# Kernel tuning notes

Hardware: AMD Instinct MI355X
Metric: run time of the kernel (lower is better)

The kernel has to match this reference:

```python
import jax, jax.numpy as jnp
import numpy as np

SEQ_LEN = 252
FEAT = 21
HID = 128


def setup_inputs() -> dict:
    key = jax.random.key(0)
    ks = jax.random.split(key, 20)
    B = 4096
    values = jax.random.normal(ks[0], (B, SEQ_LEN, FEAT), jnp.float32)
    masks = (jax.random.uniform(ks[1], (B, SEQ_LEN, FEAT)) < 0.8).astype(jnp.float32)
    deltas = jax.random.uniform(ks[2], (B, SEQ_LEN, FEAT), jnp.float32)
    evals = jax.random.normal(ks[3], (B, SEQ_LEN, FEAT), jnp.float32)
    eval_masks = (jax.random.uniform(ks[4], (B, SEQ_LEN, FEAT)) < 0.2).astype(jnp.float32)
    labels = jax.random.normal(ks[5], (B, 1), jnp.float32)
    is_train = (jax.random.uniform(ks[6], (B, 1)) < 0.8).astype(jnp.float32)
    sd = 1.0 / np.sqrt(HID)
    u = lambda k, sh, s: jax.random.uniform(k, sh, jnp.float32, -s, s)
    W_decay = u(ks[7], (HID, FEAT), sd)
    b_decay = u(ks[8], (HID,), sd)
    W_reg = u(ks[9], (FEAT, HID), sd)
    b_reg = u(ks[10], (FEAT,), sd)
    W_ih = u(ks[11], (4 * HID, 2 * FEAT), sd)
    W_hh = u(ks[12], (4 * HID, HID), sd)
    b_ih = u(ks[13], (4 * HID,), sd)
    b_hh = u(ks[14], (4 * HID,), sd)
    W_out = u(ks[15], (1, HID), sd)
    b_out = u(ks[16], (1,), sd)
    return dict(values=values, masks=masks, deltas=deltas, evals=evals,
                eval_masks=eval_masks, labels=labels, is_train=is_train,
                W_decay=W_decay, b_decay=b_decay, W_reg=W_reg, b_reg=b_reg,
                W_ih=W_ih, W_hh=W_hh, b_ih=b_ih, b_hh=b_hh,
                W_out=W_out, b_out=b_out)


def reference(values, masks, deltas, evals, eval_masks, labels, is_train,
              W_decay, b_decay, W_reg, b_reg, W_ih, W_hh, b_ih, b_hh,
              W_out, b_out):
    B = values.shape[0]
    impute_weight, label_weight = 1.0, 1.0
    # time-major [T,B,F] for scan
    xs = (jnp.swapaxes(values, 0, 1), jnp.swapaxes(masks, 0, 1),
          jnp.swapaxes(deltas, 0, 1))
    h0 = jnp.zeros((B, HID), values.dtype)
    c0 = jnp.zeros((B, HID), values.dtype)

    def step(carry, xt):
        h, c, x_loss = carry
        x, m, d = xt
        gamma = jnp.exp(-jax.nn.relu(d @ W_decay.T + b_decay))  # [B,HID]
        h = h * gamma
        x_h = h @ W_reg.T + b_reg                                # [B,FEAT]
        x_c = m * x + (1.0 - m) * x_h
        x_loss = x_loss + jnp.sum(jnp.abs(x - x_h) * m) / (jnp.sum(m) + 1e-5)
        inp = jnp.concatenate([x_c, m], axis=1)                  # [B,2*FEAT]
        gates = inp @ W_ih.T + b_ih + h @ W_hh.T + b_hh          # [B,4*HID]
        i, f, g, o = jnp.split(gates, 4, axis=1)
        c = jax.nn.sigmoid(f) * c + jax.nn.sigmoid(i) * jnp.tanh(g)
        h = jax.nn.sigmoid(o) * jnp.tanh(c)
        return (h, c, x_loss), x_c

    (h, c, x_loss), imp = jax.lax.scan(step, (h0, c0, jnp.float32(0.0)), xs)
    imputations = jnp.swapaxes(imp, 0, 1)                        # [B,T,FEAT]
    y_h = h @ W_out.T + b_out                                    # [B,1]
    y_loss = jnp.sum((y_h - labels) ** 2 * is_train) / (jnp.sum(is_train) + 1e-5)
    loss = x_loss * impute_weight + y_loss * label_weight
    return loss, y_h, imputations
```

## Files before the change

### kernel.cpp

```cpp
#include <hip/hip_runtime.h>
#include <math.h>


#define T_LEN 252
#define FEAT  21
#define HID   128
#define BTOT  4096
#define BT    16
#define NB    (BTOT / BT)
#define NTHR  512
#define LOG2E 1.44269504088896f

#define WS_WHH2   0
#define WS_RDEN   65536
#define WS_XL     65792
#define WS_YNUM   66048
#define WS_YDEN   66304

typedef __attribute__((ext_vector_type(8))) short s16x8;
typedef __attribute__((ext_vector_type(4))) float f32x4;

#define MFMA16(A, B, C) __builtin_amdgcn_mfma_f32_16x16x32_bf16((A), (B), (C), 0, 0, 0)

__device__ __forceinline__ float exp2_f(float x) { return __builtin_amdgcn_exp2f(x); }
__device__ __forceinline__ float rcp_f(float x)  { return __builtin_amdgcn_rcpf(x); }
__device__ __forceinline__ unsigned short to_bf16(float x) {
    unsigned int u = __float_as_uint(x);
    return (unsigned short)((u + 0x7FFFu + ((u >> 16) & 1u)) >> 16);
}
__device__ __forceinline__ unsigned short to_bf16f(float x) {
    return (unsigned short)((__float_as_uint(x) + 0x8000u) >> 16);
}

__global__ __launch_bounds__(1024) void rits_den(
    const float* __restrict__ masks, float* __restrict__ rden)
{
    const int t = blockIdx.x;
    const int tid = threadIdx.x;
    __shared__ float red[1024];
    float acc = 0.0f;
    if (tid < 48 * FEAT) {
        int r0 = tid / FEAT, f = tid - r0 * FEAT;
        for (int r = r0; r < BTOT; r += 48)
            acc += masks[r * (T_LEN * FEAT) + t * FEAT + f];
    }
    red[tid] = acc;
    __syncthreads();
    #pragma unroll
    for (int s = 512; s > 0; s >>= 1) {
        if (tid < s) red[tid] += red[tid + s];
        __syncthreads();
    }
    if (tid == 0) rden[t] = 1.0f / (red[0] + 1e-5f);
}

__global__ __launch_bounds__(256) void rits_fold(
    const float* __restrict__ W_ih, const float* __restrict__ W_hh,
    const float* __restrict__ W_reg, float* __restrict__ whh2)
{
    int idx = blockIdx.x * 256 + threadIdx.x;
    int j4 = idx >> 7, k = idx & (HID - 1);
    float acc = W_hh[j4 * HID + k];
    #pragma unroll
    for (int f = 0; f < FEAT; ++f)
        acc += W_ih[j4 * (2 * FEAT) + f] * W_reg[f * HID + k];
    whh2[idx] = acc;
}

__global__ __launch_bounds__(NTHR, 2) void rits_main(
    const float* __restrict__ values, const float* __restrict__ masks,
    const float* __restrict__ deltas,
    const float* __restrict__ labels, const float* __restrict__ is_train,
    const float* __restrict__ W_decay, const float* __restrict__ b_decay,
    const float* __restrict__ W_reg, const float* __restrict__ b_reg,
    const float* __restrict__ W_ih, const float* __restrict__ W_hh,
    const float* __restrict__ b_ih, const float* __restrict__ b_hh,
    const float* __restrict__ W_out, const float* __restrict__ b_out,
    const float* __restrict__ whh2, const float* __restrict__ rden,
    float* __restrict__ out_yh,
    float* __restrict__ out_imp,
    float* __restrict__ xlpart, float* __restrict__ wsynum, float* __restrict__ wsyden)
{
    const int tid  = threadIdx.x;
    const int blk  = blockIdx.x;
    const int bbase = blk * BT;
    const int l    = tid & 63;
    const int wv   = tid >> 6;
    const int cidx = l & 15;
    const int gidx = l >> 4;
    const int jh   = 16 * wv + cidx;

    __shared__ unsigned short ak_s[2][BT][200];
    __shared__ unsigned short d_s[2][BT][40];
    __shared__ float2 xm_s[2][BT][22];
    __shared__ float hfin_s[BT][HID + 4];
    __shared__ float rden_s[T_LEN];
    __shared__ float red_s[NTHR];

    for (int i = tid; i < 2 * BT * 200; i += NTHR) ((unsigned short*)ak_s)[i] = 0;
    for (int i = tid; i < 2 * BT * 40;  i += NTHR) ((unsigned short*)d_s)[i] = 0;
    if (tid < T_LEN) rden_s[tid] = rden[tid];

    s16x8 bfr_g[4][6];
    float bs_r[4];
    #pragma unroll
    for (int g = 0; g < 4; ++g) {
        const float sg = (g == 2) ? (2.0f * LOG2E) : LOG2E;
        const float* rh2 = whh2 + (g * HID + jh) * HID;
        const float* rih = W_ih + (g * HID + jh) * (2 * FEAT);
        #pragma unroll
        for (int s = 0; s < 6; ++s) {
            s16x8 fr;
            #pragma unroll
            for (int j = 0; j < 8; ++j) {
                int k = 32 * s + 8 * gidx + j;
                float w;
                if (k < HID)       w = rh2[k];
                else if (k < 160)  w = (k - 128 < FEAT) ? rih[k - 128] : 0.0f;
                else               w = (k - 160 < FEAT) ? rih[FEAT + (k - 160)] : 0.0f;
                fr[j] = (short)to_bf16(w * sg);
            }
            bfr_g[g][s] = fr;
        }
        float bb = b_ih[g * HID + jh] + b_hh[g * HID + jh];
        #pragma unroll
        for (int f = 0; f < FEAT; ++f) bb += rih[f] * b_reg[f];
        bs_r[g] = bb * sg;
    }
    s16x8 bfr_d;
    {
        const float* rw = W_decay + jh * FEAT;
        #pragma unroll
        for (int j = 0; j < 8; ++j) {
            int f = 8 * gidx + j;
            bfr_d[j] = (short)to_bf16(f < FEAT ? rw[f] * LOG2E : 0.0f);
        }
    }
    const float bd_r = b_decay[jh] * LOG2E;
    const int  fx  = 16 * wv + cidx;
    const bool fxv = (wv < 2) && (fx < FEAT);
    const int  fxc = fxv ? fx : 0;
    s16x8 bfr_r[4];
    #pragma unroll
    for (int s = 0; s < 4; ++s) {
        s16x8 fr;
        #pragma unroll
        for (int j = 0; j < 8; ++j) {
            int k = 32 * s + 8 * gidx + j;
            fr[j] = (short)to_bf16(fxv ? W_reg[fxc * HID + k] : 0.0f);
        }
        bfr_r[s] = fr;
    }
    const float br_r = fxv ? b_reg[fxc] : 0.0f;
    __syncthreads();

    const int st  = tid - 128;
    const bool stg = (st >= 0) && (st < BT * FEAT);
    const int rr = stg ? st / FEAT : 0;
    const int ff = stg ? (st - rr * FEAT) : 0;
    const int rowbase = (bbase + rr) * (T_LEN * FEAT) + ff;
    float nx = 0.f, nm = 0.f, nd = 0.f;
    if (stg) {
        float x0 = values[rowbase], m0 = masks[rowbase];
        xm_s[0][rr][ff] = make_float2(x0, m0);
        ak_s[0][rr][160 + ff] = to_bf16(m0);
        nx = values[rowbase + FEAT];
        nm = masks[rowbase + FEAT];
        nd = deltas[rowbase + FEAT];
    }
    const int ibase = (bbase + 4 * gidx) * (T_LEN * FEAT) + fxc;
    float c_r[4]   = {0.f, 0.f, 0.f, 0.f};
    float h_r[4]   = {0.f, 0.f, 0.f, 0.f};
    float gam_r[4] = {0.f, 0.f, 0.f, 0.f};
    float xl_acc = 0.0f;
    __syncthreads();

    for (int t = 0; t < T_LEN; ++t) {
        const int par = t & 1;

        float lx = 0.f, lm = 0.f, ld = 0.f;
        if (stg) {
            d_s[par ^ 1][rr][ff] = to_bf16f(nd);
            xm_s[par ^ 1][rr][ff] = make_float2(nx, nm);
            int idx = (t + 2 < T_LEN) ? (t + 2) : (T_LEN - 1);
            int o = rowbase + idx * FEAT;
            lx = values[o]; lm = masks[o]; ld = deltas[o];
        }
        #pragma unroll
        for (int v = 0; v < 4; ++v)
            ak_s[par][4 * gidx + v][jh] = to_bf16f(h_r[v] * gam_r[v]);
        __syncthreads();

        s16x8 aF0 = *(const s16x8*)&ak_s[par][cidx][      8 * gidx];
        s16x8 aF1 = *(const s16x8*)&ak_s[par][cidx][ 32 + 8 * gidx];
        s16x8 aF2 = *(const s16x8*)&ak_s[par][cidx][ 64 + 8 * gidx];
        s16x8 aF3 = *(const s16x8*)&ak_s[par][cidx][ 96 + 8 * gidx];
        s16x8 aM  = *(const s16x8*)&ak_s[par][cidx][160 + 8 * gidx];
        s16x8 ad  = *(const s16x8*)&d_s[par ^ 1][cidx][8 * gidx];
        if (stg) ak_s[par ^ 1][rr][160 + ff] = to_bf16f(nm);

        f32x4 acc0 = {bs_r[0], bs_r[0], bs_r[0], bs_r[0]};
        f32x4 acc1 = {bs_r[1], bs_r[1], bs_r[1], bs_r[1]};
        f32x4 acc2 = {bs_r[2], bs_r[2], bs_r[2], bs_r[2]};
        f32x4 acc3 = {bs_r[3], bs_r[3], bs_r[3], bs_r[3]};
        acc0 = MFMA16(aF0, bfr_g[0][0], acc0); acc1 = MFMA16(aF0, bfr_g[1][0], acc1);
        acc2 = MFMA16(aF0, bfr_g[2][0], acc2); acc3 = MFMA16(aF0, bfr_g[3][0], acc3);
        acc0 = MFMA16(aF1, bfr_g[0][1], acc0); acc1 = MFMA16(aF1, bfr_g[1][1], acc1);
        acc2 = MFMA16(aF1, bfr_g[2][1], acc2); acc3 = MFMA16(aF1, bfr_g[3][1], acc3);
        acc0 = MFMA16(aF2, bfr_g[0][2], acc0); acc1 = MFMA16(aF2, bfr_g[1][2], acc1);
        acc2 = MFMA16(aF2, bfr_g[2][2], acc2); acc3 = MFMA16(aF2, bfr_g[3][2], acc3);
        acc0 = MFMA16(aF3, bfr_g[0][3], acc0); acc1 = MFMA16(aF3, bfr_g[1][3], acc1);
        acc2 = MFMA16(aF3, bfr_g[2][3], acc2); acc3 = MFMA16(aF3, bfr_g[3][3], acc3);
        acc0 = MFMA16(aM, bfr_g[0][5], acc0);  acc1 = MFMA16(aM, bfr_g[1][5], acc1);
        acc2 = MFMA16(aM, bfr_g[2][5], acc2);  acc3 = MFMA16(aM, bfr_g[3][5], acc3);
        f32x4 gacc = {bd_r, bd_r, bd_r, bd_r};
        gacc = MFMA16(ad, bfr_d, gacc);

        if (wv < 2) {
            f32x4 xacc = {br_r, br_r, br_r, br_r};
            xacc = MFMA16(aF0, bfr_r[0], xacc);
            xacc = MFMA16(aF1, bfr_r[1], xacc);
            xacc = MFMA16(aF2, bfr_r[2], xacc);
            xacc = MFMA16(aF3, bfr_r[3], xacc);
            if (fxv) {
                const float rd = rden_s[t];
                #pragma unroll
                for (int v = 0; v < 4; ++v) {
                    float2 xm = xm_s[par][4 * gidx + v][fxc];
                    float xh = xacc[v];
                    float e  = xm.y * (xm.x - xh);
                    ak_s[par][4 * gidx + v][128 + fxc] = to_bf16f(e);
                    out_imp[ibase + v * (T_LEN * FEAT) + t * FEAT] = xh + e;
                    xl_acc += fabsf(xm.x - xh) * xm.y * rd;
                }
            }
        }
        if (stg) { nx = lx; nm = lm; nd = ld; }
        __syncthreads();

        s16x8 aE = *(const s16x8*)&ak_s[par][cidx][128 + 8 * gidx];
        acc0 = MFMA16(aE, bfr_g[0][4], acc0);
        acc1 = MFMA16(aE, bfr_g[1][4], acc1);
        acc2 = MFMA16(aE, bfr_g[2][4], acc2);
        acc3 = MFMA16(aE, bfr_g[3][4], acc3);
        #pragma unroll
        for (int v = 0; v < 4; ++v) {
            float ig = rcp_f(1.0f + exp2_f(-acc0[v]));
            float fg = rcp_f(1.0f + exp2_f(-acc1[v]));
            float gg = 2.0f * rcp_f(1.0f + exp2_f(-acc2[v])) - 1.0f;
            float og = rcp_f(1.0f + exp2_f(-acc3[v]));
            c_r[v] = fg * c_r[v] + ig * gg;
            float th = 2.0f * rcp_f(1.0f + exp2_f(-2.0f * LOG2E * c_r[v])) - 1.0f;
            h_r[v] = og * th;
            gam_r[v] = exp2_f(-fmaxf(gacc[v], 0.0f));
        }
    }

    #pragma unroll
    for (int v = 0; v < 4; ++v) hfin_s[4 * gidx + v][jh] = h_r[v];
    red_s[tid] = xl_acc;
    __syncthreads();
    #pragma unroll
    for (int s = NTHR / 2; s > 0; s >>= 1) {
        if (tid < s) red_s[tid] += red_s[tid + s];
        __syncthreads();
    }
    if (tid == 0) xlpart[blk] = red_s[0];

    float yerr = 0.0f, ytr = 0.0f;
    if (tid < BT) {
        float acc = b_out[0];
        for (int k = 0; k < HID; ++k) acc += W_out[k] * hfin_s[tid][k];
        out_yh[bbase + tid] = acc;
        float it = is_train[bbase + tid];
        float dv = acc - labels[bbase + tid];
        yerr = dv * dv * it;
        ytr  = it;
    }
    #pragma unroll
    for (int s = 8; s > 0; s >>= 1) {
        yerr += __shfl_down(yerr, s);
        ytr  += __shfl_down(ytr, s);
    }
    if (tid == 0) { wsynum[blk] = yerr; wsyden[blk] = ytr; }
}

__global__ __launch_bounds__(256) void rits_final(
    const float* __restrict__ xlpart,
    const float* __restrict__ wsynum, const float* __restrict__ wsyden,
    float* __restrict__ d_out)
{
    __shared__ float sx[256], sy[256], sz[256];
    int tid = threadIdx.x;
    sx[tid] = xlpart[tid];
    sy[tid] = wsynum[tid];
    sz[tid] = wsyden[tid];
    __syncthreads();
    for (int s = 128; s > 0; s >>= 1) {
        if (tid < s) { sx[tid] += sx[tid + s]; sy[tid] += sy[tid + s]; sz[tid] += sz[tid + s]; }
        __syncthreads();
    }
    if (tid == 0) d_out[0] = sx[0] + sy[0] / (sz[0] + 1e-5f);
}

extern "C" void kernel_launch(void* const* d_in, const int* in_sizes, int n_in,
                              void* d_out, int out_size, void* d_ws, size_t ws_size,
                              hipStream_t stream)
{
    const float* values    = (const float*)d_in[0];
    const float* masks     = (const float*)d_in[1];
    const float* deltas    = (const float*)d_in[2];
    const float* labels    = (const float*)d_in[5];
    const float* is_train  = (const float*)d_in[6];
    const float* W_decay   = (const float*)d_in[7];
    const float* b_decay   = (const float*)d_in[8];
    const float* W_reg     = (const float*)d_in[9];
    const float* b_reg     = (const float*)d_in[10];
    const float* W_ih      = (const float*)d_in[11];
    const float* W_hh      = (const float*)d_in[12];
    const float* b_ih      = (const float*)d_in[13];
    const float* b_hh      = (const float*)d_in[14];
    const float* W_out     = (const float*)d_in[15];
    const float* b_out     = (const float*)d_in[16];

    float* ws     = (float*)d_ws;
    float* whh2   = ws + WS_WHH2;
    float* rden   = ws + WS_RDEN;
    float* xlpart = ws + WS_XL;
    float* wsynum = ws + WS_YNUM;
    float* wsyden = ws + WS_YDEN;

    float* out     = (float*)d_out;
    float* out_yh  = out + 1;
    float* out_imp = out + 1 + BTOT;

    rits_den<<<dim3(T_LEN), dim3(1024), 0, stream>>>(masks, rden);
    rits_fold<<<dim3(256), dim3(256), 0, stream>>>(W_ih, W_hh, W_reg, whh2);

    rits_main<<<dim3(NB), dim3(NTHR), 0, stream>>>(
        values, masks, deltas, labels, is_train,
        W_decay, b_decay, W_reg, b_reg, W_ih, W_hh, b_ih, b_hh, W_out, b_out,
        whh2, rden, out_yh, out_imp, xlpart, wsynum, wsyden);

    rits_final<<<dim3(1), dim3(256), 0, stream>>>(xlpart, wsynum, wsyden, out);
}
```

Measured before the change: 422.5 us.

## Compute regression redundantly per wave to drop second per-step barrier

Every wave now computes the full x_h regression with two MFMA tiles and writes its own error values into a private per-wave LDS scratch. It then reads them back for the input-gate MFMA, so the second __syncthreads per timestep is gone. The x/m staging buffer becomes triple-buffered to stay safe with only one barrier per step, and the mask/error K-slots are reorganised. The cost is eight extra MFMAs per wave per step and more LDS and registers, in exchange for shortening the serial critical path.

```diff
diff --git a/kernel.cpp b/kernel.cpp
--- a/kernel.cpp
+++ b/kernel.cpp
@@ -92,16 +92,18 @@
 
     __shared__ unsigned short ak_s[2][BT][200];
     __shared__ unsigned short d_s[2][BT][40];
-    __shared__ float2 xm_s[2][BT][22];
+    __shared__ float2 xm_s[3][BT][22];
+    __shared__ unsigned short escr_s[8][BT][40];
     __shared__ float hfin_s[BT][HID + 4];
     __shared__ float rden_s[T_LEN];
     __shared__ float red_s[NTHR];
 
     for (int i = tid; i < 2 * BT * 200; i += NTHR) ((unsigned short*)ak_s)[i] = 0;
     for (int i = tid; i < 2 * BT * 40;  i += NTHR) ((unsigned short*)d_s)[i] = 0;
+    for (int i = tid; i < 8 * BT * 40;  i += NTHR) ((unsigned short*)escr_s)[i] = 0;
     if (tid < T_LEN) rden_s[tid] = rden[tid];
 
-    s16x8 bfr_g[4][6];
+    s16x8 bfr_g[4][5], bfr_e[4];
     float bs_r[4];
     #pragma unroll
     for (int g = 0; g < 4; ++g) {
@@ -109,18 +111,30 @@
         const float* rh2 = whh2 + (g * HID + jh) * HID;
         const float* rih = W_ih + (g * HID + jh) * (2 * FEAT);
         #pragma unroll
-        for (int s = 0; s < 6; ++s) {
+        for (int s = 0; s < 4; ++s) {
             s16x8 fr;
             #pragma unroll
+            for (int j = 0; j < 8; ++j)
+                fr[j] = (short)to_bf16(rh2[32 * s + 8 * gidx + j] * sg);
+            bfr_g[g][s] = fr;
+        }
+        {
+            s16x8 fr;
+            #pragma unroll
             for (int j = 0; j < 8; ++j) {
-                int k = 32 * s + 8 * gidx + j;
-                float w;
-                if (k < HID)       w = rh2[k];
-                else if (k < 160)  w = (k - 128 < FEAT) ? rih[k - 128] : 0.0f;
-                else               w = (k - 160 < FEAT) ? rih[FEAT + (k - 160)] : 0.0f;
-                fr[j] = (short)to_bf16(w * sg);
-            }
-            bfr_g[g][s] = fr;
+                int fm = 8 * gidx + j;
+                fr[j] = (short)to_bf16(fm < FEAT ? rih[FEAT + fm] * sg : 0.0f);
+            }
+            bfr_g[g][4] = fr;
+        }
+        {
+            s16x8 fr;
+            #pragma unroll
+            for (int j = 0; j < 8; ++j) {
+                int f = 8 * gidx + j;
+                fr[j] = (short)to_bf16(f < FEAT ? rih[f] * sg : 0.0f);
+            }
+            bfr_e[g] = fr;
         }
         float bb = b_ih[g * HID + jh] + b_hh[g * HID + jh];
         #pragma unroll
@@ -137,21 +151,21 @@
         }
     }
     const float bd_r = b_decay[jh] * LOG2E;
-    const int  fx  = 16 * wv + cidx;
-    const bool fxv = (wv < 2) && (fx < FEAT);
-    const int  fxc = fxv ? fx : 0;
-    s16x8 bfr_r[4];
+    s16x8 bfr_xA[4], bfr_xB[4];
+    const bool fBv = (cidx < FEAT - 16);
     #pragma unroll
     for (int s = 0; s < 4; ++s) {
-        s16x8 fr;
+        s16x8 fa, fb;
         #pragma unroll
         for (int j = 0; j < 8; ++j) {
             int k = 32 * s + 8 * gidx + j;
-            fr[j] = (short)to_bf16(fxv ? W_reg[fxc * HID + k] : 0.0f);
-        }
-        bfr_r[s] = fr;
-    }
-    const float br_r = fxv ? b_reg[fxc] : 0.0f;
+            fa[j] = (short)to_bf16(W_reg[cidx * HID + k]);
+            fb[j] = (short)to_bf16(fBv ? W_reg[(16 + cidx) * HID + k] : 0.0f);
+        }
+        bfr_xA[s] = fa; bfr_xB[s] = fb;
+    }
+    const float brA = b_reg[cidx];
+    const float brB = fBv ? b_reg[16 + cidx] : 0.0f;
     __syncthreads();
 
     const int st  = tid - 128;
@@ -163,25 +177,27 @@
     if (stg) {
         float x0 = values[rowbase], m0 = masks[rowbase];
         xm_s[0][rr][ff] = make_float2(x0, m0);
-        ak_s[0][rr][160 + ff] = to_bf16(m0);
+        ak_s[0][rr][128 + ff] = to_bf16(m0);
         nx = values[rowbase + FEAT];
         nm = masks[rowbase + FEAT];
         nd = deltas[rowbase + FEAT];
     }
-    const int ibase = (bbase + 4 * gidx) * (T_LEN * FEAT) + fxc;
+    const int ibase = (bbase + 4 * gidx) * (T_LEN * FEAT);
     float c_r[4]   = {0.f, 0.f, 0.f, 0.f};
     float h_r[4]   = {0.f, 0.f, 0.f, 0.f};
     float gam_r[4] = {0.f, 0.f, 0.f, 0.f};
     float xl_acc = 0.0f;
     __syncthreads();
 
+    int bufw = 1;
+    int bufr = 0;
     for (int t = 0; t < T_LEN; ++t) {
         const int par = t & 1;
 
         float lx = 0.f, lm = 0.f, ld = 0.f;
         if (stg) {
             d_s[par ^ 1][rr][ff] = to_bf16f(nd);
-            xm_s[par ^ 1][rr][ff] = make_float2(nx, nm);
+            xm_s[bufw][rr][ff] = make_float2(nx, nm);
             int idx = (t + 2 < T_LEN) ? (t + 2) : (T_LEN - 1);
             int o = rowbase + idx * FEAT;
             lx = values[o]; lm = masks[o]; ld = deltas[o];
@@ -195,9 +211,30 @@
         s16x8 aF1 = *(const s16x8*)&ak_s[par][cidx][ 32 + 8 * gidx];
         s16x8 aF2 = *(const s16x8*)&ak_s[par][cidx][ 64 + 8 * gidx];
         s16x8 aF3 = *(const s16x8*)&ak_s[par][cidx][ 96 + 8 * gidx];
-        s16x8 aM  = *(const s16x8*)&ak_s[par][cidx][160 + 8 * gidx];
+        s16x8 aM  = *(const s16x8*)&ak_s[par][cidx][128 + 8 * gidx];
         s16x8 ad  = *(const s16x8*)&d_s[par ^ 1][cidx][8 * gidx];
-        if (stg) ak_s[par ^ 1][rr][160 + ff] = to_bf16f(nm);
+        if (stg) ak_s[par ^ 1][rr][128 + ff] = to_bf16f(nm);
+
+        f32x4 xaccA = {brA, brA, brA, brA};
+        f32x4 xaccB = {brB, brB, brB, brB};
+        xaccA = MFMA16(aF0, bfr_xA[0], xaccA); xaccB = MFMA16(aF0, bfr_xB[0], xaccB);
+        xaccA = MFMA16(aF1, bfr_xA[1], xaccA); xaccB = MFMA16(aF1, bfr_xB[1], xaccB);
+        xaccA = MFMA16(aF2, bfr_xA[2], xaccA); xaccB = MFMA16(aF2, bfr_xB[2], xaccB);
+        xaccA = MFMA16(aF3, bfr_xA[3], xaccA); xaccB = MFMA16(aF3, bfr_xB[3], xaccB);
+
+        const float rd = rden_s[t];
+        float eA[4], eB[4];
+        #pragma unroll
+        for (int v = 0; v < 4; ++v) {
+            float2 xm = xm_s[bufr][4 * gidx + v][cidx];
+            eA[v] = xm.y * (xm.x - xaccA[v]);
+            escr_s[wv][4 * gidx + v][cidx] = to_bf16f(eA[v]);
+            if (fBv) {
+                float2 xb = xm_s[bufr][4 * gidx + v][16 + cidx];
+                eB[v] = xb.y * (xb.x - xaccB[v]);
+                escr_s[wv][4 * gidx + v][16 + cidx] = to_bf16f(eB[v]);
+            }
+        }
 
         f32x4 acc0 = {bs_r[0], bs_r[0], bs_r[0], bs_r[0]};
         f32x4 acc1 = {bs_r[1], bs_r[1], bs_r[1], bs_r[1]};
@@ -211,38 +248,33 @@
         acc2 = MFMA16(aF2, bfr_g[2][2], acc2); acc3 = MFMA16(aF2, bfr_g[3][2], acc3);
         acc0 = MFMA16(aF3, bfr_g[0][3], acc0); acc1 = MFMA16(aF3, bfr_g[1][3], acc1);
         acc2 = MFMA16(aF3, bfr_g[2][3], acc2); acc3 = MFMA16(aF3, bfr_g[3][3], acc3);
-        acc0 = MFMA16(aM, bfr_g[0][5], acc0);  acc1 = MFMA16(aM, bfr_g[1][5], acc1);
-        acc2 = MFMA16(aM, bfr_g[2][5], acc2);  acc3 = MFMA16(aM, bfr_g[3][5], acc3);
+        acc0 = MFMA16(aM, bfr_g[0][4], acc0);  acc1 = MFMA16(aM, bfr_g[1][4], acc1);
+        acc2 = MFMA16(aM, bfr_g[2][4], acc2);  acc3 = MFMA16(aM, bfr_g[3][4], acc3);
         f32x4 gacc = {bd_r, bd_r, bd_r, bd_r};
         gacc = MFMA16(ad, bfr_d, gacc);
 
-        if (wv < 2) {
-            f32x4 xacc = {br_r, br_r, br_r, br_r};
-            xacc = MFMA16(aF0, bfr_r[0], xacc);
-            xacc = MFMA16(aF1, bfr_r[1], xacc);
-            xacc = MFMA16(aF2, bfr_r[2], xacc);
-            xacc = MFMA16(aF3, bfr_r[3], xacc);
-            if (fxv) {
-                const float rd = rden_s[t];
-                #pragma unroll
-                for (int v = 0; v < 4; ++v) {
-                    float2 xm = xm_s[par][4 * gidx + v][fxc];
-                    float xh = xacc[v];
-                    float e  = xm.y * (xm.x - xh);
-                    ak_s[par][4 * gidx + v][128 + fxc] = to_bf16f(e);
-                    out_imp[ibase + v * (T_LEN * FEAT) + t * FEAT] = xh + e;
-                    xl_acc += fabsf(xm.x - xh) * xm.y * rd;
-                }
-            }
-        }
+        if (wv == 0) {
+            #pragma unroll
+            for (int v = 0; v < 4; ++v) {
+                out_imp[ibase + v * (T_LEN * FEAT) + t * FEAT + cidx] = xaccA[v] + eA[v];
+                xl_acc += fabsf(eA[v]) * rd;
+            }
+        } else if (wv == 1 && fBv) {
+            #pragma unroll
+            for (int v = 0; v < 4; ++v) {
+                out_imp[ibase + v * (T_LEN * FEAT) + t * FEAT + 16 + cidx] = xaccB[v] + eB[v];
+                xl_acc += fabsf(eB[v]) * rd;
+            }
+        }
+
+        s16x8 eF = *(const s16x8*)&escr_s[wv][cidx][8 * gidx];
+        acc0 = MFMA16(eF, bfr_e[0], acc0);
+        acc1 = MFMA16(eF, bfr_e[1], acc1);
+        acc2 = MFMA16(eF, bfr_e[2], acc2);
+        acc3 = MFMA16(eF, bfr_e[3], acc3);
+
         if (stg) { nx = lx; nm = lm; nd = ld; }
-        __syncthreads();
-
-        s16x8 aE = *(const s16x8*)&ak_s[par][cidx][128 + 8 * gidx];
-        acc0 = MFMA16(aE, bfr_g[0][4], acc0);
-        acc1 = MFMA16(aE, bfr_g[1][4], acc1);
-        acc2 = MFMA16(aE, bfr_g[2][4], acc2);
-        acc3 = MFMA16(aE, bfr_g[3][4], acc3);
+
         #pragma unroll
         for (int v = 0; v < 4; ++v) {
             float ig = rcp_f(1.0f + exp2_f(-acc0[v]));
@@ -254,6 +286,8 @@
             h_r[v] = og * th;
             gam_r[v] = exp2_f(-fmaxf(gacc[v], 0.0f));
         }
+        int nb = bufw + 1; bufw = (nb > 2) ? 0 : nb;
+        int nr = bufr + 1; bufr = (nr > 2) ? 0 : nr;
     }
 
     #pragma unroll
```

New measurement: 499.9 us. +18.3%, slower.

## Defer imputation stores to staging threads and split MFMA accumulation chains

Applied to the files above, without the earlier changes.

Imputed values are written to a shared buffer, and the staging threads store them to global memory one step later in coalesced row order. The loss term is rebuilt from the bf16-rounded error kept in shared memory instead of the full-precision value. The gate and regression MFMA chains are split into two independent accumulators to shorten dependency latency, and the time loop is unrolled by two. The aim is to take scattered global stores and long serial MFMA chains off the critical path of the two lanes that compute the regression, at the cost of a small loss-precision change and extra shared memory.

```diff
diff --git a/kernel.cpp b/kernel.cpp
--- a/kernel.cpp
+++ b/kernel.cpp
@@ -30,6 +30,9 @@
 }
 __device__ __forceinline__ unsigned short to_bf16f(float x) {
     return (unsigned short)((__float_as_uint(x) + 0x8000u) >> 16);
+}
+__device__ __forceinline__ float bf16_to_f(unsigned short u) {
+    return __uint_as_float(((unsigned int)u) << 16);
 }
 
 __global__ __launch_bounds__(1024) void rits_den(
@@ -93,6 +96,7 @@
     __shared__ unsigned short ak_s[2][BT][200];
     __shared__ unsigned short d_s[2][BT][40];
     __shared__ float2 xm_s[2][BT][22];
+    __shared__ float xc_s[2][BT][22];
     __shared__ float hfin_s[BT][HID + 4];
     __shared__ float rden_s[T_LEN];
     __shared__ float red_s[NTHR];
@@ -109,18 +113,30 @@
         const float* rh2 = whh2 + (g * HID + jh) * HID;
         const float* rih = W_ih + (g * HID + jh) * (2 * FEAT);
         #pragma unroll
-        for (int s = 0; s < 6; ++s) {
+        for (int s = 0; s < 4; ++s) {
+            s16x8 fr;
+            #pragma unroll
+            for (int j = 0; j < 8; ++j)
+                fr[j] = (short)to_bf16(rh2[32 * s + 8 * gidx + j] * sg);
+            bfr_g[g][s] = fr;
+        }
+        {
             s16x8 fr;
             #pragma unroll
             for (int j = 0; j < 8; ++j) {
-                int k = 32 * s + 8 * gidx + j;
-                float w;
-                if (k < HID)       w = rh2[k];
-                else if (k < 160)  w = (k - 128 < FEAT) ? rih[k - 128] : 0.0f;
-                else               w = (k - 160 < FEAT) ? rih[FEAT + (k - 160)] : 0.0f;
-                fr[j] = (short)to_bf16(w * sg);
+                int f = 8 * gidx + j;
+                fr[j] = (short)to_bf16(f < FEAT ? rih[f] * sg : 0.0f);
             }
-            bfr_g[g][s] = fr;
+            bfr_g[g][4] = fr;
+        }
+        {
+            s16x8 fr;
+            #pragma unroll
+            for (int j = 0; j < 8; ++j) {
+                int fm = 8 * gidx + j;
+                fr[j] = (short)to_bf16(fm < FEAT ? rih[FEAT + fm] * sg : 0.0f);
+            }
+            bfr_g[g][5] = fr;
         }
         float bb = b_ih[g * HID + jh] + b_hh[g * HID + jh];
         #pragma unroll
@@ -168,13 +184,13 @@
         nm = masks[rowbase + FEAT];
         nd = deltas[rowbase + FEAT];
     }
-    const int ibase = (bbase + 4 * gidx) * (T_LEN * FEAT) + fxc;
     float c_r[4]   = {0.f, 0.f, 0.f, 0.f};
     float h_r[4]   = {0.f, 0.f, 0.f, 0.f};
     float gam_r[4] = {0.f, 0.f, 0.f, 0.f};
     float xl_acc = 0.0f;
     __syncthreads();
 
+    #pragma unroll 2
     for (int t = 0; t < T_LEN; ++t) {
         const int par = t & 1;
 
@@ -197,41 +213,52 @@
         s16x8 aF3 = *(const s16x8*)&ak_s[par][cidx][ 96 + 8 * gidx];
         s16x8 aM  = *(const s16x8*)&ak_s[par][cidx][160 + 8 * gidx];
         s16x8 ad  = *(const s16x8*)&d_s[par ^ 1][cidx][8 * gidx];
-        if (stg) ak_s[par ^ 1][rr][160 + ff] = to_bf16f(nm);
-
-        f32x4 acc0 = {bs_r[0], bs_r[0], bs_r[0], bs_r[0]};
-        f32x4 acc1 = {bs_r[1], bs_r[1], bs_r[1], bs_r[1]};
-        f32x4 acc2 = {bs_r[2], bs_r[2], bs_r[2], bs_r[2]};
-        f32x4 acc3 = {bs_r[3], bs_r[3], bs_r[3], bs_r[3]};
-        acc0 = MFMA16(aF0, bfr_g[0][0], acc0); acc1 = MFMA16(aF0, bfr_g[1][0], acc1);
-        acc2 = MFMA16(aF0, bfr_g[2][0], acc2); acc3 = MFMA16(aF0, bfr_g[3][0], acc3);
-        acc0 = MFMA16(aF1, bfr_g[0][1], acc0); acc1 = MFMA16(aF1, bfr_g[1][1], acc1);
-        acc2 = MFMA16(aF1, bfr_g[2][1], acc2); acc3 = MFMA16(aF1, bfr_g[3][1], acc3);
-        acc0 = MFMA16(aF2, bfr_g[0][2], acc0); acc1 = MFMA16(aF2, bfr_g[1][2], acc1);
-        acc2 = MFMA16(aF2, bfr_g[2][2], acc2); acc3 = MFMA16(aF2, bfr_g[3][2], acc3);
-        acc0 = MFMA16(aF3, bfr_g[0][3], acc0); acc1 = MFMA16(aF3, bfr_g[1][3], acc1);
-        acc2 = MFMA16(aF3, bfr_g[2][3], acc2); acc3 = MFMA16(aF3, bfr_g[3][3], acc3);
-        acc0 = MFMA16(aM, bfr_g[0][5], acc0);  acc1 = MFMA16(aM, bfr_g[1][5], acc1);
-        acc2 = MFMA16(aM, bfr_g[2][5], acc2);  acc3 = MFMA16(aM, bfr_g[3][5], acc3);
+        if (stg) {
+            ak_s[par ^ 1][rr][160 + ff] = to_bf16f(nm);
+            if (t > 0) {
+                float xcp = xc_s[par ^ 1][rr][ff];
+                float ep  = bf16_to_f(ak_s[par ^ 1][rr][128 + ff]);
+                out_imp[rowbase + (t - 1) * FEAT] = xcp;
+                xl_acc += fabsf(ep) * rden_s[t - 1];
+            }
+        }
+
+        f32x4 accA0 = {bs_r[0], bs_r[0], bs_r[0], bs_r[0]};
+        f32x4 accA1 = {bs_r[1], bs_r[1], bs_r[1], bs_r[1]};
+        f32x4 accA2 = {bs_r[2], bs_r[2], bs_r[2], bs_r[2]};
+        f32x4 accA3 = {bs_r[3], bs_r[3], bs_r[3], bs_r[3]};
+        f32x4 accB0 = {0.f, 0.f, 0.f, 0.f};
+        f32x4 accB1 = {0.f, 0.f, 0.f, 0.f};
+        f32x4 accB2 = {0.f, 0.f, 0.f, 0.f};
+        f32x4 accB3 = {0.f, 0.f, 0.f, 0.f};
+        accA0 = MFMA16(aF0, bfr_g[0][0], accA0); accA1 = MFMA16(aF0, bfr_g[1][0], accA1);
+        accA2 = MFMA16(aF0, bfr_g[2][0], accA2); accA3 = MFMA16(aF0, bfr_g[3][0], accA3);
+        accB0 = MFMA16(aF2, bfr_g[0][2], accB0); accB1 = MFMA16(aF2, bfr_g[1][2], accB1);
+        accB2 = MFMA16(aF2, bfr_g[2][2], accB2); accB3 = MFMA16(aF2, bfr_g[3][2], accB3);
+        accA0 = MFMA16(aF1, bfr_g[0][1], accA0); accA1 = MFMA16(aF1, bfr_g[1][1], accA1);
+        accA2 = MFMA16(aF1, bfr_g[2][1], accA2); accA3 = MFMA16(aF1, bfr_g[3][1], accA3);
+        accB0 = MFMA16(aF3, bfr_g[0][3], accB0); accB1 = MFMA16(aF3, bfr_g[1][3], accB1);
+        accB2 = MFMA16(aF3, bfr_g[2][3], accB2); accB3 = MFMA16(aF3, bfr_g[3][3], accB3);
+        accA0 = MFMA16(aM, bfr_g[0][5], accA0);  accA1 = MFMA16(aM, bfr_g[1][5], accA1);
+        accA2 = MFMA16(aM, bfr_g[2][5], accA2);  accA3 = MFMA16(aM, bfr_g[3][5], accA3);
         f32x4 gacc = {bd_r, bd_r, bd_r, bd_r};
         gacc = MFMA16(ad, bfr_d, gacc);
 
         if (wv < 2) {
-            f32x4 xacc = {br_r, br_r, br_r, br_r};
-            xacc = MFMA16(aF0, bfr_r[0], xacc);
-            xacc = MFMA16(aF1, bfr_r[1], xacc);
-            xacc = MFMA16(aF2, bfr_r[2], xacc);
-            xacc = MFMA16(aF3, bfr_r[3], xacc);
+            f32x4 x1 = {br_r, br_r, br_r, br_r};
+            f32x4 x2 = {0.f, 0.f, 0.f, 0.f};
+            x1 = MFMA16(aF0, bfr_r[0], x1);
+            x2 = MFMA16(aF2, bfr_r[2], x2);
+            x1 = MFMA16(aF1, bfr_r[1], x1);
+            x2 = MFMA16(aF3, bfr_r[3], x2);
             if (fxv) {
-                const float rd = rden_s[t];
                 #pragma unroll
                 for (int v = 0; v < 4; ++v) {
+                    float xh = x1[v] + x2[v];
                     float2 xm = xm_s[par][4 * gidx + v][fxc];
-                    float xh = xacc[v];
                     float e  = xm.y * (xm.x - xh);
                     ak_s[par][4 * gidx + v][128 + fxc] = to_bf16f(e);
-                    out_imp[ibase + v * (T_LEN * FEAT) + t * FEAT] = xh + e;
-                    xl_acc += fabsf(xm.x - xh) * xm.y * rd;
+                    xc_s[par][4 * gidx + v][fxc] = xh + e;
                 }
             }
         }
@@ -239,21 +266,32 @@
         __syncthreads();
 
         s16x8 aE = *(const s16x8*)&ak_s[par][cidx][128 + 8 * gidx];
-        acc0 = MFMA16(aE, bfr_g[0][4], acc0);
-        acc1 = MFMA16(aE, bfr_g[1][4], acc1);
-        acc2 = MFMA16(aE, bfr_g[2][4], acc2);
-        acc3 = MFMA16(aE, bfr_g[3][4], acc3);
+        accB0 = MFMA16(aE, bfr_g[0][4], accB0);
+        accB1 = MFMA16(aE, bfr_g[1][4], accB1);
+        accB2 = MFMA16(aE, bfr_g[2][4], accB2);
+        accB3 = MFMA16(aE, bfr_g[3][4], accB3);
         #pragma unroll
         for (int v = 0; v < 4; ++v) {
-            float ig = rcp_f(1.0f + exp2_f(-acc0[v]));
-            float fg = rcp_f(1.0f + exp2_f(-acc1[v]));
-            float gg = 2.0f * rcp_f(1.0f + exp2_f(-acc2[v])) - 1.0f;
-            float og = rcp_f(1.0f + exp2_f(-acc3[v]));
+            float g0 = accA0[v] + accB0[v];
+            float g1 = accA1[v] + accB1[v];
+            float g2 = accA2[v] + accB2[v];
+            float g3 = accA3[v] + accB3[v];
+            float ig = rcp_f(1.0f + exp2_f(-g0));
+            float fg = rcp_f(1.0f + exp2_f(-g1));
+            float gg = 2.0f * rcp_f(1.0f + exp2_f(-g2)) - 1.0f;
+            float og = rcp_f(1.0f + exp2_f(-g3));
             c_r[v] = fg * c_r[v] + ig * gg;
             float th = 2.0f * rcp_f(1.0f + exp2_f(-2.0f * LOG2E * c_r[v])) - 1.0f;
             h_r[v] = og * th;
             gam_r[v] = exp2_f(-fmaxf(gacc[v], 0.0f));
         }
+    }
+
+    if (stg) {
+        float xcp = xc_s[1][rr][ff];
+        float ep  = bf16_to_f(ak_s[1][rr][128 + ff]);
+        out_imp[rowbase + (T_LEN - 1) * FEAT] = xcp;
+        xl_acc += fabsf(ep) * rden_s[T_LEN - 1];
     }
 
     #pragma unroll
```

After: 400.8 us (median of 2 runs). -5.1%, faster.
